# Kernel tuning notes

Hardware: AMD Instinct MI355X
Metric: run time of the kernel (lower is better)

## Reference

```python
import jax, jax.numpy as jnp
import numpy as np

N_NODES = 100000
N_EDGES = 1600000
IN_CH = 128
HID = 64
OUT = 10
N_GRAPHS = 64


def gcn_conv(x, W, b, row, col, n):
    # PyG GCNConv: xw = x @ W; add self-loops (weight 1);
    # deg = scatter_add(weight, col); norm = d^-1/2[row] * d^-1/2[col];
    # out[col] += norm * xw[row]; out += b
    xw = x @ W  # [N, out_ch]
    loop = jnp.arange(n, dtype=row.dtype)
    r = jnp.concatenate([row, loop])
    c = jnp.concatenate([col, loop])
    deg = jax.ops.segment_sum(jnp.ones_like(c, dtype=xw.dtype), c, num_segments=n)
    dis = jnp.where(deg > 0, jax.lax.rsqrt(deg), 0.0)
    norm = dis[r] * dis[c]  # [E+N]
    msgs = norm[:, None] * xw[r]  # gather + scale
    agg = jax.ops.segment_sum(msgs, c, num_segments=n)  # scatter-add
    return agg + b


def global_mean_pool(x, batch, num_graphs):
    sums = jax.ops.segment_sum(x, batch, num_segments=num_graphs)
    cnt = jax.ops.segment_sum(jnp.ones((x.shape[0],), x.dtype), batch, num_segments=num_graphs)
    return sums / jnp.maximum(cnt, 1.0)[:, None]


def setup_inputs() -> dict:
    key = jax.random.key(0)
    ks = jax.random.split(key, 9)
    x = jax.random.normal(ks[0], (N_NODES, IN_CH), dtype=jnp.float32)
    edge_index = jax.random.randint(ks[1], (2, N_EDGES), 0, N_NODES, dtype=jnp.int64)
    batch = jnp.sort(jax.random.randint(ks[2], (N_NODES,), 0, N_GRAPHS, dtype=jnp.int64))
    def glorot(k, shape):
        lim = np.sqrt(6.0 / (shape[0] + shape[1]))
        return jax.random.uniform(k, shape, jnp.float32, -lim, lim)
    W1 = glorot(ks[3], (IN_CH, HID)); b1 = jnp.zeros((HID,), jnp.float32)
    W2 = glorot(ks[4], (HID, HID)); b2 = jnp.zeros((HID,), jnp.float32)
    Wl = glorot(ks[5], (HID, OUT)); bl = jnp.zeros((OUT,), jnp.float32)
    return {"x": x, "W1": W1, "b1": b1, "W2": W2, "b2": b2,
            "Wl": Wl, "bl": bl, "edge_index": edge_index, "batch": batch}


def reference(x, W1, b1, W2, b2, Wl, bl, edge_index, batch):
    row, col = edge_index[0], edge_index[1]
    n = x.shape[0]
    h = jax.nn.relu(gcn_conv(x, W1, b1, row, col, n))
    h = jax.nn.relu(gcn_conv(h, W2, b2, row, col, n))
    g = global_mean_pool(h, batch, N_GRAPHS)  # [G, HID]
    return g @ Wl + bl  # [G, OUT]
```

## Files before the change

### kernel.cpp

```cpp
#include <hip/hip_runtime.h>


static __device__ inline ushort f32_to_bf16_rne(float f) {
    uint32_t u = __float_as_uint(f);
    uint32_t r = (u + 0x7fffu + ((u >> 16) & 1u)) >> 16;
    return (ushort)r;
}
static __device__ inline float bf_lo(uint32_t u) { return __uint_as_float(u << 16); }
static __device__ inline float bf_hi(uint32_t u) { return __uint_as_float(u & 0xffff0000u); }

__global__ __launch_bounds__(256) void deg_kernel(const int* __restrict__ col,
                                                  int* __restrict__ deg, int E) {
    int e = blockIdx.x * 256 + threadIdx.x;
    if (e < E) atomicAdd(&deg[col[e]], 1);
}

__global__ __launch_bounds__(512) void block_sum_kernel(const int* __restrict__ deg,
                                                        int* __restrict__ bsums, int n) {
    __shared__ int sm[512];
    int i = blockIdx.x * 512 + threadIdx.x;
    sm[threadIdx.x] = (i < n) ? deg[i] : 0;
    __syncthreads();
    for (int s = 256; s > 0; s >>= 1) {
        if (threadIdx.x < s) sm[threadIdx.x] += sm[threadIdx.x + s];
        __syncthreads();
    }
    if (threadIdx.x == 0) bsums[blockIdx.x] = sm[0];
}

__global__ __launch_bounds__(256) void scan_bsums_kernel(int* __restrict__ bsums, int nb) {
    __shared__ int sm[256];
    int v = (threadIdx.x < nb) ? bsums[threadIdx.x] : 0;
    sm[threadIdx.x] = v;
    __syncthreads();
    for (int off = 1; off < 256; off <<= 1) {
        int t = (threadIdx.x >= off) ? sm[threadIdx.x - off] : 0;
        __syncthreads();
        sm[threadIdx.x] += t;
        __syncthreads();
    }
    if (threadIdx.x < nb) bsums[threadIdx.x] = sm[threadIdx.x] - v;
}

__global__ __launch_bounds__(512) void scan_write_kernel(const int* __restrict__ deg,
                                                         const int* __restrict__ bsums,
                                                         int* __restrict__ rowptr,
                                                         float* __restrict__ dis,
                                                         int n, int E) {
    __shared__ int sm[512];
    int i = blockIdx.x * 512 + threadIdx.x;
    int v = (i < n) ? deg[i] : 0;
    sm[threadIdx.x] = v;
    __syncthreads();
    for (int off = 1; off < 512; off <<= 1) {
        int t = (threadIdx.x >= off) ? sm[threadIdx.x - off] : 0;
        __syncthreads();
        sm[threadIdx.x] += t;
        __syncthreads();
    }
    if (i < n) {
        rowptr[i] = bsums[blockIdx.x] + sm[threadIdx.x] - v;
        dis[i] = rsqrtf((float)v + 1.0f);
    }
    if (blockIdx.x == 0 && threadIdx.x == 0) rowptr[n] = E;
}

template <int K>
__device__ __forceinline__ void gemm_tile_body(const float* __restrict__ x,
                                               const float* __restrict__ W,
                                               ushort* __restrict__ out, int n, int bx) {
    __shared__ float As[32][64];
    __shared__ float Ws[32 * 64];
    const int tid = threadIdx.x;
    const int tr = tid >> 4;
    const int tc = tid & 15;
    const int base = bx * 64;

    float acc[4][4];
#pragma unroll
    for (int i = 0; i < 4; ++i)
#pragma unroll
        for (int j = 0; j < 4; ++j) acc[i][j] = 0.0f;

    const int tnode = tid >> 3;
    const int tk4 = (tid & 7) * 4;

    for (int kc = 0; kc < K; kc += 32) {
        __syncthreads();
#pragma unroll
        for (int h = 0; h < 2; ++h) {
            int m = tnode + h * 32;
            int node = base + m;
            float4 v = make_float4(0.f, 0.f, 0.f, 0.f);
            if (node < n) v = *(const float4*)&x[(size_t)node * K + kc + tk4];
            As[tk4 + 0][m] = v.x; As[tk4 + 1][m] = v.y;
            As[tk4 + 2][m] = v.z; As[tk4 + 3][m] = v.w;
        }
#pragma unroll
        for (int r = 0; r < 2; ++r) {
            int o = tid * 4 + r * 1024;
            *(float4*)&Ws[o] = *(const float4*)&W[kc * 64 + o];
        }
        __syncthreads();
#pragma unroll
        for (int k = 0; k < 32; ++k) {
            float4 a = *(const float4*)&As[k][tr * 4];
            float4 b = *(const float4*)&Ws[k * 64 + tc * 4];
            const float av[4] = {a.x, a.y, a.z, a.w};
            const float bv[4] = {b.x, b.y, b.z, b.w};
#pragma unroll
            for (int i = 0; i < 4; ++i)
#pragma unroll
                for (int j = 0; j < 4; ++j)
                    acc[i][j] = fmaf(av[i], bv[j], acc[i][j]);
        }
    }
#pragma unroll
    for (int i = 0; i < 4; ++i) {
        int node = base + tr * 4 + i;
        if (node < n) {
            ushort4 st;
            st.x = f32_to_bf16_rne(acc[i][0]);
            st.y = f32_to_bf16_rne(acc[i][1]);
            st.z = f32_to_bf16_rne(acc[i][2]);
            st.w = f32_to_bf16_rne(acc[i][3]);
            *(ushort4*)&out[(size_t)node * 64 + tc * 4] = st;
        }
    }
}

template <int K>
__global__ __launch_bounds__(256) void gemm_tiled(const float* __restrict__ x,
                                                  const float* __restrict__ W,
                                                  ushort* __restrict__ out, int n) {
    gemm_tile_body<K>(x, W, out, n, blockIdx.x);
}

template <int K>
__global__ __launch_bounds__(256) void fused_fill_gemm(
        const float* __restrict__ x, const float* __restrict__ W,
        ushort* __restrict__ out, int n, int nb_fill,
        const int* __restrict__ row, const int* __restrict__ col,
        const int* __restrict__ rowptr, int* __restrict__ fill,
        int* __restrict__ csrs, int E) {
    if ((int)blockIdx.x >= nb_fill) {
        gemm_tile_body<K>(x, W, out, n, blockIdx.x - nb_fill);
        return;
    }
    const int stride = nb_fill * 256;
    for (int e = blockIdx.x * 256 + threadIdx.x; e < E; e += stride) {
        int r = row[e], c = col[e];
        int pos = rowptr[c] + atomicAdd(&fill[c], 1);
        csrs[pos] = r;
    }
}

template <int OUT_BF16>
__global__ __launch_bounds__(256) void gcn_pull_kernel(const ushort* __restrict__ xw,
                                                       const int* __restrict__ csrs,
                                                       const int* __restrict__ rowptr,
                                                       const float* __restrict__ dis,
                                                       const float* __restrict__ b,
                                                       void* __restrict__ outv, int n) {
    const int lane = threadIdx.x & 63;
    const int wid = threadIdx.x >> 6;
    const int half = lane >> 5;
    const int q = lane & 31;
    const float2 bb = ((const float2*)b)[q];

    for (int i = blockIdx.x * 4 + wid; i < n; i += gridDim.x * 4) {
        int s = rowptr[i], t = rowptr[i + 1];
        float di = dis[i];
        float ax = 0.0f, ay = 0.0f;
        if (half == 0) {
            uint32_t u = *(const uint32_t*)(xw + ((size_t)i << 6) + (q << 1));
            ax = di * bf_lo(u);
            ay = di * bf_hi(u);
        }
        int e = s + half;
        for (; e + 6 < t; e += 8) {
            int s0 = csrs[e], s1 = csrs[e + 2], s2 = csrs[e + 4], s3 = csrs[e + 6];
            float d0 = dis[s0], d1 = dis[s1], d2 = dis[s2], d3 = dis[s3];
            uint32_t u0 = *(const uint32_t*)(xw + ((size_t)s0 << 6) + (q << 1));
            uint32_t u1 = *(const uint32_t*)(xw + ((size_t)s1 << 6) + (q << 1));
            uint32_t u2 = *(const uint32_t*)(xw + ((size_t)s2 << 6) + (q << 1));
            uint32_t u3 = *(const uint32_t*)(xw + ((size_t)s3 << 6) + (q << 1));
            ax = fmaf(d0, bf_lo(u0), ax); ay = fmaf(d0, bf_hi(u0), ay);
            ax = fmaf(d1, bf_lo(u1), ax); ay = fmaf(d1, bf_hi(u1), ay);
            ax = fmaf(d2, bf_lo(u2), ax); ay = fmaf(d2, bf_hi(u2), ay);
            ax = fmaf(d3, bf_lo(u3), ax); ay = fmaf(d3, bf_hi(u3), ay);
        }
        for (; e + 2 < t; e += 4) {
            int s0 = csrs[e], s1 = csrs[e + 2];
            float d0 = dis[s0], d1 = dis[s1];
            uint32_t u0 = *(const uint32_t*)(xw + ((size_t)s0 << 6) + (q << 1));
            uint32_t u1 = *(const uint32_t*)(xw + ((size_t)s1 << 6) + (q << 1));
            ax = fmaf(d0, bf_lo(u0), ax); ay = fmaf(d0, bf_hi(u0), ay);
            ax = fmaf(d1, bf_lo(u1), ax); ay = fmaf(d1, bf_hi(u1), ay);
        }
        for (; e < t; e += 2) {
            int s0 = csrs[e];
            float d0 = dis[s0];
            uint32_t u0 = *(const uint32_t*)(xw + ((size_t)s0 << 6) + (q << 1));
            ax = fmaf(d0, bf_lo(u0), ax); ay = fmaf(d0, bf_hi(u0), ay);
        }
        ax += __shfl_xor(ax, 32);
        ay += __shfl_xor(ay, 32);
        if (half == 0) {
            float v0 = fmaxf(fmaf(di, ax, bb.x), 0.0f);
            float v1 = fmaxf(fmaf(di, ay, bb.y), 0.0f);
            if (OUT_BF16) {
                ushort2 st = make_ushort2(f32_to_bf16_rne(v0), f32_to_bf16_rne(v1));
                *(ushort2*)((ushort*)outv + ((size_t)i << 6) + (q << 1)) = st;
            } else {
                *(float2*)((float*)outv + ((size_t)i << 6) + (q << 1)) = make_float2(v0, v1);
            }
        }
    }
}

__global__ __launch_bounds__(256) void pool_kernel(const ushort* __restrict__ h,
                                                   const int* __restrict__ batch,
                                                   float* __restrict__ pool,
                                                   float* __restrict__ cnt, int n) {
    const int lane = threadIdx.x & 63;
    const int wid = threadIdx.x >> 6;
    const int start = (blockIdx.x * 4 + wid) * 32;
    const int end = min(start + 32, n);
    if (start >= end) return;
    int gcur = batch[start];
    float acc = 0.0f;
    int c = 0;
    for (int i = start; i < end; ++i) {
        int g = batch[i];
        if (g != gcur) {
            atomicAdd(&pool[gcur * 64 + lane], acc);
            if (lane == 0) atomicAdd(&cnt[gcur], (float)c);
            acc = 0.0f; c = 0; gcur = g;
        }
        acc += __uint_as_float((uint32_t)h[(size_t)i * 64 + lane] << 16);
        ++c;
    }
    atomicAdd(&pool[gcur * 64 + lane], acc);
    if (lane == 0) atomicAdd(&cnt[gcur], (float)c);
}

__global__ __launch_bounds__(640) void final_kernel(const float* __restrict__ pool,
                                                    const float* __restrict__ cnt,
                                                    const float* __restrict__ Wl,
                                                    const float* __restrict__ bl,
                                                    float* __restrict__ out) {
    int tid = threadIdx.x;
    int g = tid / 10, o = tid % 10;
    float inv = 1.0f / fmaxf(cnt[g], 1.0f);
    float acc = 0.0f;
#pragma unroll
    for (int l = 0; l < 64; ++l)
        acc = fmaf(pool[g * 64 + l] * inv, Wl[l * 10 + o], acc);
    out[tid] = acc + bl[o];
}

extern "C" void kernel_launch(void* const* d_in, const int* in_sizes, int n_in,
                              void* d_out, int out_size, void* d_ws, size_t ws_size,
                              hipStream_t stream) {
    const float* x  = (const float*)d_in[0];
    const float* W1 = (const float*)d_in[1];
    const float* b1 = (const float*)d_in[2];
    const float* W2 = (const float*)d_in[3];
    const float* b2 = (const float*)d_in[4];
    const float* Wl = (const float*)d_in[5];
    const float* bl = (const float*)d_in[6];
    const int*   ei = (const int*)d_in[7];
    const int*   batch = (const int*)d_in[8];
    float* out = (float*)d_out;

    const int n = in_sizes[8];
    const int E = in_sizes[7] / 2;
    const int F = 64;

    const int* row = ei;
    const int* col = ei + E;

    char* p = (char*)d_ws;
    auto alloc = [&](size_t bytes) {
        char* r = p;
        p += (bytes + 255) & ~(size_t)255;
        return r;
    };
    int*    degi   = (int*)   alloc((size_t)n * 4);
    int*    rowptr = (int*)   alloc((size_t)(n + 1) * 4);
    int*    bsums  = (int*)   alloc(256 * 4);
    float*  dis    = (float*) alloc((size_t)n * 4);
    int*    csrs   = (int*)   alloc((size_t)E * 4);
    ushort* xwB    = (ushort*)alloc((size_t)n * F * 2);
    float*  B      = (float*) alloc((size_t)n * F * 4);
    float*  pool   = (float*) alloc(64 * 64 * 4);
    float*  cnt    = (float*) alloc(64 * 4);

    const int nb_edge = (E + 255) / 256;
    const int nb_scan = (n + 511) / 512;
    const int nb_gemm = (n + 63) / 64;
    const int nb_fill = 1024;

    hipMemsetAsync(degi, 0, (size_t)n * 4, stream);
    deg_kernel<<<nb_edge, 256, 0, stream>>>(col, degi, E);
    block_sum_kernel<<<nb_scan, 512, 0, stream>>>(degi, bsums, n);
    scan_bsums_kernel<<<1, 256, 0, stream>>>(bsums, nb_scan);
    scan_write_kernel<<<nb_scan, 512, 0, stream>>>(degi, bsums, rowptr, dis, n, E);
    hipMemsetAsync(degi, 0, (size_t)n * 4, stream);

    fused_fill_gemm<128><<<nb_fill + nb_gemm, 256, 0, stream>>>(
        x, W1, xwB, n, nb_fill, row, col, rowptr, degi, csrs, E);

    gcn_pull_kernel<0><<<2048, 256, 0, stream>>>(xwB, csrs, rowptr, dis, b1, B, n);

    gemm_tiled<64><<<nb_gemm, 256, 0, stream>>>(B, W2, xwB, n);
    gcn_pull_kernel<1><<<2048, 256, 0, stream>>>(xwB, csrs, rowptr, dis, b2, B, n);

    hipMemsetAsync(pool, 0, (64 * 64 + 64) * sizeof(float), stream);
    pool_kernel<<<(n + 127) / 128, 256, 0, stream>>>((const ushort*)B, batch, pool, cnt, n);
    final_kernel<<<1, 640, 0, stream>>>(pool, cnt, Wl, bl, out);
}
```

Before: 436.7 us.

## Two-pass bucketed CSR build, prescale xw by deg^-1/2, half-wave per node pull

Result: slower. 578.8 us (+32.6%).

```diff
diff --git a/kernel.cpp b/kernel.cpp
--- a/kernel.cpp
+++ b/kernel.cpp
@@ -65,16 +65,49 @@
     if (blockIdx.x == 0 && threadIdx.x == 0) rowptr[n] = E;
 }
 
+__global__ __launch_bounds__(256) void bucket_pass1(const int* __restrict__ row,
+                                                    const int* __restrict__ col,
+                                                    const int* __restrict__ rowptr,
+                                                    int* __restrict__ bfill,
+                                                    int* __restrict__ inter, int E) {
+    int e = blockIdx.x * 256 + threadIdx.x;
+    if (e >= E) return;
+    int r = row[e], c = col[e];
+    int b = c >> 6;
+    int base = rowptr[b << 6];
+    int idx = atomicAdd(&bfill[b], 1);
+    inter[base + idx] = r | ((c & 63) << 26);
+}
+
+__global__ __launch_bounds__(256) void bucket_pass2(const int* __restrict__ inter,
+                                                    const int* __restrict__ rowptr,
+                                                    int* __restrict__ csrs, int n) {
+    __shared__ int lcnt[64];
+    const int nb0 = blockIdx.x << 6;
+    const int nend = min(nb0 + 64, n);
+    const int s = rowptr[nb0], t = rowptr[nend];
+    if (threadIdx.x < 64) lcnt[threadIdx.x] = 0;
+    __syncthreads();
+    for (int e = s + threadIdx.x; e < t; e += 256) {
+        int w = inter[e];
+        int r = w & 0x03FFFFFF;
+        int clow = (int)((unsigned)w >> 26);
+        int pos = rowptr[nb0 + clow] + atomicAdd(&lcnt[clow], 1);
+        csrs[pos] = r;
+    }
+}
+
 template <int K>
-__device__ __forceinline__ void gemm_tile_body(const float* __restrict__ x,
-                                               const float* __restrict__ W,
-                                               ushort* __restrict__ out, int n, int bx) {
-    __shared__ float As[32][64];
+__global__ __launch_bounds__(256) void gemm_tiled(const float* __restrict__ x,
+                                                  const float* __restrict__ W,
+                                                  const float* __restrict__ dis,
+                                                  ushort* __restrict__ out, int n) {
+    __shared__ float As[32][68];
     __shared__ float Ws[32 * 64];
     const int tid = threadIdx.x;
     const int tr = tid >> 4;
     const int tc = tid & 15;
-    const int base = bx * 64;
+    const int base = blockIdx.x * 64;
 
     float acc[4][4];
 #pragma unroll
@@ -119,103 +152,77 @@
     for (int i = 0; i < 4; ++i) {
         int node = base + tr * 4 + i;
         if (node < n) {
+            float d = dis[node];
             ushort4 st;
-            st.x = f32_to_bf16_rne(acc[i][0]);
-            st.y = f32_to_bf16_rne(acc[i][1]);
-            st.z = f32_to_bf16_rne(acc[i][2]);
-            st.w = f32_to_bf16_rne(acc[i][3]);
+            st.x = f32_to_bf16_rne(acc[i][0] * d);
+            st.y = f32_to_bf16_rne(acc[i][1] * d);
+            st.z = f32_to_bf16_rne(acc[i][2] * d);
+            st.w = f32_to_bf16_rne(acc[i][3] * d);
             *(ushort4*)&out[(size_t)node * 64 + tc * 4] = st;
         }
     }
 }
 
-template <int K>
-__global__ __launch_bounds__(256) void gemm_tiled(const float* __restrict__ x,
-                                                  const float* __restrict__ W,
-                                                  ushort* __restrict__ out, int n) {
-    gemm_tile_body<K>(x, W, out, n, blockIdx.x);
-}
-
-template <int K>
-__global__ __launch_bounds__(256) void fused_fill_gemm(
-        const float* __restrict__ x, const float* __restrict__ W,
-        ushort* __restrict__ out, int n, int nb_fill,
-        const int* __restrict__ row, const int* __restrict__ col,
-        const int* __restrict__ rowptr, int* __restrict__ fill,
-        int* __restrict__ csrs, int E) {
-    if ((int)blockIdx.x >= nb_fill) {
-        gemm_tile_body<K>(x, W, out, n, blockIdx.x - nb_fill);
-        return;
-    }
-    const int stride = nb_fill * 256;
-    for (int e = blockIdx.x * 256 + threadIdx.x; e < E; e += stride) {
-        int r = row[e], c = col[e];
-        int pos = rowptr[c] + atomicAdd(&fill[c], 1);
-        csrs[pos] = r;
-    }
-}
-
 template <int OUT_BF16>
-__global__ __launch_bounds__(256) void gcn_pull_kernel(const ushort* __restrict__ xw,
+__global__ __launch_bounds__(256) void gcn_pull_kernel(const ushort* __restrict__ xws,
                                                        const int* __restrict__ csrs,
                                                        const int* __restrict__ rowptr,
                                                        const float* __restrict__ dis,
                                                        const float* __restrict__ b,
                                                        void* __restrict__ outv, int n) {
     const int lane = threadIdx.x & 63;
-    const int wid = threadIdx.x >> 6;
+    const int wv = threadIdx.x >> 6;
     const int half = lane >> 5;
     const int q = lane & 31;
     const float2 bb = ((const float2*)b)[q];
 
-    for (int i = blockIdx.x * 4 + wid; i < n; i += gridDim.x * 4) {
-        int s = rowptr[i], t = rowptr[i + 1];
-        float di = dis[i];
-        float ax = 0.0f, ay = 0.0f;
-        if (half == 0) {
-            uint32_t u = *(const uint32_t*)(xw + ((size_t)i << 6) + (q << 1));
-            ax = di * bf_lo(u);
-            ay = di * bf_hi(u);
-        }
-        int e = s + half;
-        for (; e + 6 < t; e += 8) {
-            int s0 = csrs[e], s1 = csrs[e + 2], s2 = csrs[e + 4], s3 = csrs[e + 6];
-            float d0 = dis[s0], d1 = dis[s1], d2 = dis[s2], d3 = dis[s3];
-            uint32_t u0 = *(const uint32_t*)(xw + ((size_t)s0 << 6) + (q << 1));
-            uint32_t u1 = *(const uint32_t*)(xw + ((size_t)s1 << 6) + (q << 1));
-            uint32_t u2 = *(const uint32_t*)(xw + ((size_t)s2 << 6) + (q << 1));
-            uint32_t u3 = *(const uint32_t*)(xw + ((size_t)s3 << 6) + (q << 1));
-            ax = fmaf(d0, bf_lo(u0), ax); ay = fmaf(d0, bf_hi(u0), ay);
-            ax = fmaf(d1, bf_lo(u1), ax); ay = fmaf(d1, bf_hi(u1), ay);
-            ax = fmaf(d2, bf_lo(u2), ax); ay = fmaf(d2, bf_hi(u2), ay);
-            ax = fmaf(d3, bf_lo(u3), ax); ay = fmaf(d3, bf_hi(u3), ay);
-        }
-        for (; e + 2 < t; e += 4) {
-            int s0 = csrs[e], s1 = csrs[e + 2];
-            float d0 = dis[s0], d1 = dis[s1];
-            uint32_t u0 = *(const uint32_t*)(xw + ((size_t)s0 << 6) + (q << 1));
-            uint32_t u1 = *(const uint32_t*)(xw + ((size_t)s1 << 6) + (q << 1));
-            ax = fmaf(d0, bf_lo(u0), ax); ay = fmaf(d0, bf_hi(u0), ay);
-            ax = fmaf(d1, bf_lo(u1), ax); ay = fmaf(d1, bf_hi(u1), ay);
-        }
-        for (; e < t; e += 2) {
-            int s0 = csrs[e];
-            float d0 = dis[s0];
-            uint32_t u0 = *(const uint32_t*)(xw + ((size_t)s0 << 6) + (q << 1));
-            ax = fmaf(d0, bf_lo(u0), ax); ay = fmaf(d0, bf_hi(u0), ay);
-        }
-        ax += __shfl_xor(ax, 32);
-        ay += __shfl_xor(ay, 32);
-        if (half == 0) {
-            float v0 = fmaxf(fmaf(di, ax, bb.x), 0.0f);
-            float v1 = fmaxf(fmaf(di, ay, bb.y), 0.0f);
-            if (OUT_BF16) {
-                ushort2 st = make_ushort2(f32_to_bf16_rne(v0), f32_to_bf16_rne(v1));
-                *(ushort2*)((ushort*)outv + ((size_t)i << 6) + (q << 1)) = st;
-            } else {
-                *(float2*)((float*)outv + ((size_t)i << 6) + (q << 1)) = make_float2(v0, v1);
-            }
-        }
+    const int i = (blockIdx.x * 4 + wv) * 2 + half;
+    if (i >= n) return;
+
+    const int s = rowptr[i], t = rowptr[i + 1];
+    uint32_t us = *(const uint32_t*)(xws + ((size_t)i << 6) + (q << 1));
+    float ax = bf_lo(us), ay = bf_hi(us);
+    int e = s;
+    for (; e + 8 <= t; e += 8) {
+        int s0 = csrs[e + 0], s1 = csrs[e + 1], s2 = csrs[e + 2], s3 = csrs[e + 3];
+        int s4 = csrs[e + 4], s5 = csrs[e + 5], s6 = csrs[e + 6], s7 = csrs[e + 7];
+        uint32_t u0 = *(const uint32_t*)(xws + ((size_t)s0 << 6) + (q << 1));
+        uint32_t u1 = *(const uint32_t*)(xws + ((size_t)s1 << 6) + (q << 1));
+        uint32_t u2 = *(const uint32_t*)(xws + ((size_t)s2 << 6) + (q << 1));
+        uint32_t u3 = *(const uint32_t*)(xws + ((size_t)s3 << 6) + (q << 1));
+        uint32_t u4 = *(const uint32_t*)(xws + ((size_t)s4 << 6) + (q << 1));
+        uint32_t u5 = *(const uint32_t*)(xws + ((size_t)s5 << 6) + (q << 1));
+        uint32_t u6 = *(const uint32_t*)(xws + ((size_t)s6 << 6) + (q << 1));
+        uint32_t u7 = *(const uint32_t*)(xws + ((size_t)s7 << 6) + (q << 1));
+        ax += bf_lo(u0); ay += bf_hi(u0);
+        ax += bf_lo(u1); ay += bf_hi(u1);
+        ax += bf_lo(u2); ay += bf_hi(u2);
+        ax += bf_lo(u3); ay += bf_hi(u3);
+        ax += bf_lo(u4); ay += bf_hi(u4);
+        ax += bf_lo(u5); ay += bf_hi(u5);
+        ax += bf_lo(u6); ay += bf_hi(u6);
+        ax += bf_lo(u7); ay += bf_hi(u7);
+    }
+    for (; e + 2 <= t; e += 2) {
+        int s0 = csrs[e], s1 = csrs[e + 1];
+        uint32_t u0 = *(const uint32_t*)(xws + ((size_t)s0 << 6) + (q << 1));
+        uint32_t u1 = *(const uint32_t*)(xws + ((size_t)s1 << 6) + (q << 1));
+        ax += bf_lo(u0); ay += bf_hi(u0);
+        ax += bf_lo(u1); ay += bf_hi(u1);
+    }
+    if (e < t) {
+        int s0 = csrs[e];
+        uint32_t u0 = *(const uint32_t*)(xws + ((size_t)s0 << 6) + (q << 1));
+        ax += bf_lo(u0); ay += bf_hi(u0);
+    }
+    const float di = dis[i];
+    float v0 = fmaxf(fmaf(di, ax, bb.x), 0.0f);
+    float v1 = fmaxf(fmaf(di, ay, bb.y), 0.0f);
+    if (OUT_BF16) {
+        ushort2 st = make_ushort2(f32_to_bf16_rne(v0), f32_to_bf16_rne(v1));
+        *(ushort2*)((ushort*)outv + ((size_t)i << 6) + (q << 1)) = st;
+    } else {
+        *(float2*)((float*)outv + ((size_t)i << 6) + (q << 1)) = make_float2(v0, v1);
     }
 }
 
@@ -292,6 +299,7 @@
     int*    bsums  = (int*)   alloc(256 * 4);
     float*  dis    = (float*) alloc((size_t)n * 4);
     int*    csrs   = (int*)   alloc((size_t)E * 4);
+    int*    inter  = (int*)   alloc((size_t)E * 4);
     ushort* xwB    = (ushort*)alloc((size_t)n * F * 2);
     float*  B      = (float*) alloc((size_t)n * F * 4);
     float*  pool   = (float*) alloc(64 * 64 * 4);
@@ -300,22 +308,22 @@
     const int nb_edge = (E + 255) / 256;
     const int nb_scan = (n + 511) / 512;
     const int nb_gemm = (n + 63) / 64;
-    const int nb_fill = 1024;
+    const int nbuck   = (n + 63) / 64;
 
     hipMemsetAsync(degi, 0, (size_t)n * 4, stream);
     deg_kernel<<<nb_edge, 256, 0, stream>>>(col, degi, E);
     block_sum_kernel<<<nb_scan, 512, 0, stream>>>(degi, bsums, n);
     scan_bsums_kernel<<<1, 256, 0, stream>>>(bsums, nb_scan);
     scan_write_kernel<<<nb_scan, 512, 0, stream>>>(degi, bsums, rowptr, dis, n, E);
-    hipMemsetAsync(degi, 0, (size_t)n * 4, stream);
-
-    fused_fill_gemm<128><<<nb_fill + nb_gemm, 256, 0, stream>>>(
-        x, W1, xwB, n, nb_fill, row, col, rowptr, degi, csrs, E);
-
-    gcn_pull_kernel<0><<<2048, 256, 0, stream>>>(xwB, csrs, rowptr, dis, b1, B, n);
-
-    gemm_tiled<64><<<nb_gemm, 256, 0, stream>>>(B, W2, xwB, n);
-    gcn_pull_kernel<1><<<2048, 256, 0, stream>>>(xwB, csrs, rowptr, dis, b2, B, n);
+    hipMemsetAsync(degi, 0, (size_t)nbuck * 4, stream);
+    bucket_pass1<<<nb_edge, 256, 0, stream>>>(row, col, rowptr, degi, inter, E);
+    bucket_pass2<<<nbuck, 256, 0, stream>>>(inter, rowptr, csrs, n);
+
+    gemm_tiled<128><<<nb_gemm, 256, 0, stream>>>(x, W1, dis, xwB, n);
+    gcn_pull_kernel<0><<<(n + 7) / 8, 256, 0, stream>>>(xwB, csrs, rowptr, dis, b1, B, n);
+
+    gemm_tiled<64><<<nb_gemm, 256, 0, stream>>>(B, W2, dis, xwB, n);
+    gcn_pull_kernel<1><<<(n + 7) / 8, 256, 0, stream>>>(xwB, csrs, rowptr, dis, b2, B, n);
 
     hipMemsetAsync(pool, 0, (64 * 64 + 64) * sizeof(float), stream);
     pool_kernel<<<(n + 127) / 128, 256, 0, stream>>>((const ushort*)B, batch, pool, cnt, n);
```
